# Performance work log

Hardware: AMD Instinct MI355X
Metric: run time of the kernel (lower is better)

Reference implementation:

```python
import jax, jax.numpy as jnp
import numpy as np

PADDING_IDX = 0


def setup_inputs() -> dict:
    key = jax.random.key(0)
    k1, k2 = jax.random.split(key)
    B, S, D = 64, 2048, 128
    V = 200000
    grad_output = jax.random.normal(k1, (B, S, D), dtype=jnp.float32)
    indices = jax.random.randint(k2, (B, S), 0, V, dtype=jnp.int64)
    return {"grad_output": grad_output, "indices": indices, "num_embeddings": V}


def reference(grad_output, indices, num_embeddings):
    D = grad_output.shape[-1]
    flat_idx = indices.reshape(-1)                      # [B*S]
    flat_grad = grad_output.reshape(-1, D)              # [B*S, D]
    # Zero out contributions from padding positions; padding row stays 0,
    # matching the original (it never accumulates into padding_idx).
    mask = (flat_idx != PADDING_IDX)[:, None]           # [B*S, 1]
    masked_grad = jnp.where(mask, flat_grad, jnp.zeros((), dtype=flat_grad.dtype))
    dense_grad = jax.ops.segment_sum(masked_grad, flat_idx,
                                     num_segments=num_embeddings)
    return dense_grad.astype(jnp.float32)
```

## Files before the change

### kernel.cpp

```cpp
#include <hip/hip_runtime.h>


#define EMB_D   128
#define PAD_IDX 0
#define MAXC    4
#define OVF_CAP 8192

__global__ void __launch_bounds__(256)
scatter_slots(const int* __restrict__ idx, unsigned* __restrict__ counts,
              unsigned* __restrict__ slots, unsigned* __restrict__ ovfcnt,
              unsigned* __restrict__ ovf_row, unsigned* __restrict__ ovf_tok, int n) {
    int i = blockIdx.x * blockDim.x + threadIdx.x;
    if (i >= n) return;
    int e = idx[i];
    if (e == PAD_IDX) return;
    unsigned p = atomicAdd(&counts[e], 1u);
    if (p < MAXC) {
        slots[(size_t)e * MAXC + p] = (unsigned)i;
    } else {
        unsigned q = atomicAdd(ovfcnt, 1u);
        if (q < OVF_CAP) { ovf_row[q] = (unsigned)e; ovf_tok[q] = (unsigned)i; }
    }
}

__global__ void __launch_bounds__(256)
reduce_write(const float* __restrict__ grad, const unsigned* __restrict__ counts,
             const unsigned* __restrict__ slots, float* __restrict__ out, int V) {
    int wave = (blockIdx.x * 256 + (int)threadIdx.x) >> 6;
    int lane = threadIdx.x & 63;
    if (wave >= V) return;
    const int v = wave;
    const float2* __restrict__ g2 = (const float2*)grad;

    float2 a0 = make_float2(0.f, 0.f), a1 = a0, a2 = a0, a3 = a0;
    unsigned c = counts[v];
    if (v != PAD_IDX && c > 0) {
        unsigned cc = c < MAXC ? c : MAXC;
        uint4 s = ((const uint4*)slots)[v];
        if (cc > 0) a0 = g2[(size_t)s.x * (EMB_D / 2) + lane];
        if (cc > 1) a1 = g2[(size_t)s.y * (EMB_D / 2) + lane];
        if (cc > 2) a2 = g2[(size_t)s.z * (EMB_D / 2) + lane];
        if (cc > 3) a3 = g2[(size_t)s.w * (EMB_D / 2) + lane];
    }
    float2 acc;
    acc.x = (a0.x + a1.x) + (a2.x + a3.x);
    acc.y = (a0.y + a1.y) + (a2.y + a3.y);
    ((float2*)out)[(size_t)v * (EMB_D / 2) + lane] = acc;
}

__global__ void __launch_bounds__(256)
ovf_fix(const float* __restrict__ grad, const unsigned* __restrict__ ovfcnt,
        const unsigned* __restrict__ ovf_row, const unsigned* __restrict__ ovf_tok,
        float* __restrict__ out) {
    unsigned n = *ovfcnt;
    if (n > OVF_CAP) n = OVF_CAP;
    int nwaves = (gridDim.x * 256) >> 6;
    int wave = (blockIdx.x * 256 + (int)threadIdx.x) >> 6;
    int lane = threadIdx.x & 63;
    const float2* __restrict__ g2 = (const float2*)grad;
    for (unsigned e = wave; e < n; e += nwaves) {
        unsigned v = ovf_row[e], t = ovf_tok[e];
        float2 g = g2[(size_t)t * (EMB_D / 2) + lane];
        float* dst = out + (size_t)v * EMB_D + lane * 2;
        unsafeAtomicAdd(dst + 0, g.x);
        unsafeAtomicAdd(dst + 1, g.y);
    }
}

__global__ void zero_f32x4(float4* __restrict__ p, long n4) {
    long i = (long)blockIdx.x * blockDim.x + threadIdx.x;
    long stride = (long)gridDim.x * blockDim.x;
    const float4 z = make_float4(0.f, 0.f, 0.f, 0.f);
    for (; i < n4; i += stride) p[i] = z;
}

__global__ void __launch_bounds__(256)
scatter_add_kernel(const float* __restrict__ grad, const int* __restrict__ idx,
                   float* __restrict__ out, int ntok) {
    int gid = blockIdx.x * blockDim.x + threadIdx.x;
    int token = gid >> 5;
    int d4 = gid & 31;
    if (token >= ntok) return;
    int e = idx[token];
    if (e == PAD_IDX) return;
    const float4 g = ((const float4*)grad)[(size_t)token * 32 + d4];
    float* dst = out + (size_t)e * EMB_D + d4 * 4;
    unsafeAtomicAdd(dst + 0, g.x);
    unsafeAtomicAdd(dst + 1, g.y);
    unsafeAtomicAdd(dst + 2, g.z);
    unsafeAtomicAdd(dst + 3, g.w);
}

extern "C" void kernel_launch(void* const* d_in, const int* in_sizes, int n_in,
                              void* d_out, int out_size, void* d_ws, size_t ws_size,
                              hipStream_t stream) {
    const float* grad = (const float*)d_in[0];
    const int*   idx  = (const int*)d_in[1];
    float*       out  = (float*)d_out;
    const int ntok = in_sizes[1];
    const int V = out_size / EMB_D;

    size_t off_counts = 0;
    size_t off_ovfcnt = off_counts + (size_t)V * 4;
    size_t off_slots  = off_ovfcnt + 16;
    size_t off_orow   = off_slots + (size_t)V * MAXC * 4;
    size_t off_otok   = off_orow + (size_t)OVF_CAP * 4;
    size_t need       = off_otok + (size_t)OVF_CAP * 4;

    if (ws_size < need) {
        zero_f32x4<<<4096, 256, 0, stream>>>((float4*)out, (long)out_size / 4);
        const int threads = ntok * 32;
        scatter_add_kernel<<<(threads + 255) / 256, 256, 0, stream>>>(grad, idx, out, ntok);
        return;
    }

    char* ws = (char*)d_ws;
    unsigned* counts  = (unsigned*)(ws + off_counts);
    unsigned* ovfcnt  = (unsigned*)(ws + off_ovfcnt);
    unsigned* slots   = (unsigned*)(ws + off_slots);
    unsigned* ovf_row = (unsigned*)(ws + off_orow);
    unsigned* ovf_tok = (unsigned*)(ws + off_otok);

    hipMemsetAsync(counts, 0, (size_t)V * 4 + 16, stream);

    scatter_slots<<<(ntok + 255) / 256, 256, 0, stream>>>(
        idx, counts, slots, ovfcnt, ovf_row, ovf_tok, ntok);

    int nblocks = (V + 3) / 4;
    reduce_write<<<nblocks, 256, 0, stream>>>(grad, counts, slots, out, V);

    ovf_fix<<<16, 256, 0, stream>>>(grad, ovfcnt, ovf_row, ovf_tok, out);
}
```

Before: 207.2 us.

## Widen slot table, fold overflow into reduce kernel, use half-wave float4 rows

Raises per-row slot capacity from 4 to 8 and drops the separate overflow atomic kernel. Rows with more than 8 hits now scan the packed overflow list inside the reduce kernel. Each half-wave handles one row with float4 loads, and slot and output writes use nontemporal stores. This removes one kernel launch and its atomics, and issues the gathers branch-free using masks. The cost is a larger slot table, plus a serial overflow scan that is slow if many rows exceed eight hits.

After: 182.2 us. -12.1%, faster.

```diff
diff --git a/kernel.cpp b/kernel.cpp
--- a/kernel.cpp
+++ b/kernel.cpp
@@ -3,68 +3,91 @@
 
 #define EMB_D   128
 #define PAD_IDX 0
-#define MAXC    4
-#define OVF_CAP 8192
+#define MAXC    8
+#define OVF_CAP 16384
+
+typedef float fvec4 __attribute__((ext_vector_type(4)));
 
 __global__ void __launch_bounds__(256)
 scatter_slots(const int* __restrict__ idx, unsigned* __restrict__ counts,
               unsigned* __restrict__ slots, unsigned* __restrict__ ovfcnt,
-              unsigned* __restrict__ ovf_row, unsigned* __restrict__ ovf_tok, int n) {
+              uint2* __restrict__ ovf, int n) {
     int i = blockIdx.x * blockDim.x + threadIdx.x;
     if (i >= n) return;
     int e = idx[i];
     if (e == PAD_IDX) return;
     unsigned p = atomicAdd(&counts[e], 1u);
     if (p < MAXC) {
-        slots[(size_t)e * MAXC + p] = (unsigned)i;
+        __builtin_nontemporal_store((unsigned)i, &slots[(size_t)e * MAXC + p]);
     } else {
         unsigned q = atomicAdd(ovfcnt, 1u);
-        if (q < OVF_CAP) { ovf_row[q] = (unsigned)e; ovf_tok[q] = (unsigned)i; }
+        if (q < OVF_CAP) ovf[q] = make_uint2((unsigned)e, (unsigned)i);
     }
 }
 
 __global__ void __launch_bounds__(256)
 reduce_write(const float* __restrict__ grad, const unsigned* __restrict__ counts,
-             const unsigned* __restrict__ slots, float* __restrict__ out, int V) {
-    int wave = (blockIdx.x * 256 + (int)threadIdx.x) >> 6;
-    int lane = threadIdx.x & 63;
-    if (wave >= V) return;
-    const int v = wave;
-    const float2* __restrict__ g2 = (const float2*)grad;
+             const uint4* __restrict__ slots4, const unsigned* __restrict__ ovfcnt,
+             const uint2* __restrict__ ovf, float* __restrict__ out, int V) {
+    int wid  = (blockIdx.x * 256 + (int)threadIdx.x) >> 6;
+    int half = (threadIdx.x >> 5) & 1;
+    int lane = threadIdx.x & 31;
+    int v = wid * 2 + half;
+    if (v >= V) return;
 
-    float2 a0 = make_float2(0.f, 0.f), a1 = a0, a2 = a0, a3 = a0;
+    const float4* __restrict__ g4 = (const float4*)grad;
+    float4 acc = make_float4(0.f, 0.f, 0.f, 0.f);
+
     unsigned c = counts[v];
-    if (v != PAD_IDX && c > 0) {
-        unsigned cc = c < MAXC ? c : MAXC;
-        uint4 s = ((const uint4*)slots)[v];
-        if (cc > 0) a0 = g2[(size_t)s.x * (EMB_D / 2) + lane];
-        if (cc > 1) a1 = g2[(size_t)s.y * (EMB_D / 2) + lane];
-        if (cc > 2) a2 = g2[(size_t)s.z * (EMB_D / 2) + lane];
-        if (cc > 3) a3 = g2[(size_t)s.w * (EMB_D / 2) + lane];
+    if (c != 0u) {
+        uint4 s0 = slots4[(size_t)v * 2];
+        unsigned i1 = (c > 1u) ? s0.y : s0.x;
+        unsigned i2 = (c > 2u) ? s0.z : s0.x;
+        unsigned i3 = (c > 3u) ? s0.w : s0.x;
+        float4 a0 = g4[(size_t)s0.x * 32 + lane];
+        float4 a1 = g4[(size_t)i1   * 32 + lane];
+        float4 a2 = g4[(size_t)i2   * 32 + lane];
+        float4 a3 = g4[(size_t)i3   * 32 + lane];
+        float m1 = (c > 1u) ? 1.f : 0.f;
+        float m2 = (c > 2u) ? 1.f : 0.f;
+        float m3 = (c > 3u) ? 1.f : 0.f;
+        acc.x = a0.x + m1 * a1.x + m2 * a2.x + m3 * a3.x;
+        acc.y = a0.y + m1 * a1.y + m2 * a2.y + m3 * a3.y;
+        acc.z = a0.z + m1 * a1.z + m2 * a2.z + m3 * a3.z;
+        acc.w = a0.w + m1 * a1.w + m2 * a2.w + m3 * a3.w;
+
+        if (c > 4u) {
+            uint4 s1 = slots4[(size_t)v * 2 + 1];
+            unsigned j1 = (c > 5u) ? s1.y : s1.x;
+            unsigned j2 = (c > 6u) ? s1.z : s1.x;
+            unsigned j3 = (c > 7u) ? s1.w : s1.x;
+            float4 b0 = g4[(size_t)s1.x * 32 + lane];
+            float4 b1 = g4[(size_t)j1   * 32 + lane];
+            float4 b2 = g4[(size_t)j2   * 32 + lane];
+            float4 b3 = g4[(size_t)j3   * 32 + lane];
+            float n1 = (c > 5u) ? 1.f : 0.f;
+            float n2 = (c > 6u) ? 1.f : 0.f;
+            float n3 = (c > 7u) ? 1.f : 0.f;
+            acc.x += b0.x + n1 * b1.x + n2 * b2.x + n3 * b3.x;
+            acc.y += b0.y + n1 * b1.y + n2 * b2.y + n3 * b3.y;
+            acc.z += b0.z + n1 * b1.z + n2 * b2.z + n3 * b3.z;
+            acc.w += b0.w + n1 * b1.w + n2 * b2.w + n3 * b3.w;
+
+            if (c > (unsigned)MAXC) {
+                unsigned n = *ovfcnt;
+                if (n > OVF_CAP) n = OVF_CAP;
+                for (unsigned q = 0; q < n; ++q) {
+                    uint2 eo = ovf[q];
+                    if (eo.x == (unsigned)v) {
+                        float4 g = g4[(size_t)eo.y * 32 + lane];
+                        acc.x += g.x; acc.y += g.y; acc.z += g.z; acc.w += g.w;
+                    }
+                }
+            }
+        }
     }
-    float2 acc;
-    acc.x = (a0.x + a1.x) + (a2.x + a3.x);
-    acc.y = (a0.y + a1.y) + (a2.y + a3.y);
-    ((float2*)out)[(size_t)v * (EMB_D / 2) + lane] = acc;
-}
-
-__global__ void __launch_bounds__(256)
-ovf_fix(const float* __restrict__ grad, const unsigned* __restrict__ ovfcnt,
-        const unsigned* __restrict__ ovf_row, const unsigned* __restrict__ ovf_tok,
-        float* __restrict__ out) {
-    unsigned n = *ovfcnt;
-    if (n > OVF_CAP) n = OVF_CAP;
-    int nwaves = (gridDim.x * 256) >> 6;
-    int wave = (blockIdx.x * 256 + (int)threadIdx.x) >> 6;
-    int lane = threadIdx.x & 63;
-    const float2* __restrict__ g2 = (const float2*)grad;
-    for (unsigned e = wave; e < n; e += nwaves) {
-        unsigned v = ovf_row[e], t = ovf_tok[e];
-        float2 g = g2[(size_t)t * (EMB_D / 2) + lane];
-        float* dst = out + (size_t)v * EMB_D + lane * 2;
-        unsafeAtomicAdd(dst + 0, g.x);
-        unsafeAtomicAdd(dst + 1, g.y);
-    }
+    fvec4 accv = { acc.x, acc.y, acc.z, acc.w };
+    __builtin_nontemporal_store(accv, &((fvec4*)out)[(size_t)v * 32 + lane]);
 }
 
 __global__ void zero_f32x4(float4* __restrict__ p, long n4) {
@@ -103,9 +126,8 @@
     size_t off_counts = 0;
     size_t off_ovfcnt = off_counts + (size_t)V * 4;
     size_t off_slots  = off_ovfcnt + 16;
-    size_t off_orow   = off_slots + (size_t)V * MAXC * 4;
-    size_t off_otok   = off_orow + (size_t)OVF_CAP * 4;
-    size_t need       = off_otok + (size_t)OVF_CAP * 4;
+    size_t off_ovf    = off_slots + (size_t)V * MAXC * 4;
+    size_t need       = off_ovf + (size_t)OVF_CAP * 8;
 
     if (ws_size < need) {
         zero_f32x4<<<4096, 256, 0, stream>>>((float4*)out, (long)out_size / 4);
@@ -115,19 +137,18 @@
     }
 
     char* ws = (char*)d_ws;
-    unsigned* counts  = (unsigned*)(ws + off_counts);
-    unsigned* ovfcnt  = (unsigned*)(ws + off_ovfcnt);
-    unsigned* slots   = (unsigned*)(ws + off_slots);
-    unsigned* ovf_row = (unsigned*)(ws + off_orow);
-    unsigned* ovf_tok = (unsigned*)(ws + off_otok);
+    unsigned* counts = (unsigned*)(ws + off_counts);
+    unsigned* ovfcnt = (unsigned*)(ws + off_ovfcnt);
+    unsigned* slots  = (unsigned*)(ws + off_slots);
+    uint2*    ovf    = (uint2*)(ws + off_ovf);
 
-    hipMemsetAsync(counts, 0, (size_t)V * 4 + 16, stream);
+    (void)hipMemsetAsync(counts, 0, (size_t)V * 4 + 16, stream);
 
     scatter_slots<<<(ntok + 255) / 256, 256, 0, stream>>>(
-        idx, counts, slots, ovfcnt, ovf_row, ovf_tok, ntok);
+        idx, counts, slots, ovfcnt, ovf, ntok);
 
-    int nblocks = (V + 3) / 4;
-    reduce_write<<<nblocks, 256, 0, stream>>>(grad, counts, slots, out, V);
-
-    ovf_fix<<<16, 256, 0, stream>>>(grad, ovfcnt, ovf_row, ovf_tok, out);
+    int waves = (V + 1) / 2;
+    int nblocks = (waves + 3) / 4;
+    reduce_write<<<nblocks, 256, 0, stream>>>(
+        grad, counts, (const uint4*)slots, ovfcnt, ovf, out, V);
 }
```
